# Performance work log

Measured on AMD Instinct MI355X. Metric: run time of the kernel, lower is better.

## Reference

```python
import jax, jax.numpy as jnp
import numpy as np

N, E, IN_C, HID, OUT_C, L = 50000, 800000, 256, 96, 64, 3
DELTAS = (1.0, 0.5, 0.25)


def setup_inputs() -> dict:
    key = jax.random.key(0)
    ks = jax.random.split(key, 10)
    x = jax.random.normal(ks[0], (N, IN_C), dtype=jnp.float32)
    edge_index = jax.random.randint(ks[1], (2, E), 0, N, dtype=jnp.int64)
    s = 1.0 / np.sqrt(IN_C)
    proj_w = jax.random.uniform(ks[2], (IN_C, HID), jnp.float32, -s, s)
    proj_b = jax.random.uniform(ks[3], (HID,), jnp.float32, -s, s)
    sh = 1.0 / np.sqrt(HID)
    conv_w = jax.random.uniform(ks[4], (L, HID, HID), jnp.float32, -sh, sh)
    conv_b = jnp.zeros((L, HID), dtype=jnp.float32)
    so = 1.0 / np.sqrt(2 * HID)
    out_w = jax.random.uniform(ks[5], (2 * HID, OUT_C), jnp.float32, -so, so)
    out_b = jax.random.uniform(ks[6], (OUT_C,), jnp.float32, -so, so)
    # dithered-quantization uniform noise in (-0.5, 0.5), per layer
    b_noise = jax.random.uniform(ks[7], (L, N, HID), jnp.float32) - 0.5
    # additive gaussian noise, per layer
    eps_noise = jax.random.normal(ks[8], (L, N, HID), dtype=jnp.float32) * 0.01
    return {
        "x": x, "edge_index": edge_index,
        "proj_w": proj_w, "proj_b": proj_b,
        "conv_w": conv_w, "conv_b": conv_b,
        "out_w": out_w, "out_b": out_b,
        "b_noise": b_noise, "eps_noise": eps_noise,
    }


def _gcn_norm(edge_index, n):
    # add self-loops and compute symmetric normalization (PyG gcn_norm)
    loops = jnp.arange(n, dtype=edge_index.dtype)
    src = jnp.concatenate([edge_index[0], loops])
    dst = jnp.concatenate([edge_index[1], loops])
    deg = jax.ops.segment_sum(jnp.ones_like(dst, dtype=jnp.float32), dst, num_segments=n)
    dis = jnp.where(deg > 0, jax.lax.rsqrt(jnp.maximum(deg, 1.0)), 0.0)
    norm = dis[src] * dis[dst]  # [E+N]
    return src, dst, norm


def reference(x, edge_index, proj_w, proj_b, conv_w, conv_b, out_w, out_b, b_noise, eps_noise):
    n = x.shape[0]
    src, dst, norm = _gcn_norm(edge_index, n)
    h0 = x @ proj_w + proj_b  # [N, HID]
    h = h0
    for k in range(L):
        delta = DELTAS[k]
        b = b_noise[k] * delta
        h_q = jnp.floor((h + b) / delta) * delta - b  # dithered quantize
        m = h_q @ conv_w[k]                           # [N, HID]
        agg = jax.ops.segment_sum(m[src] * norm[:, None], dst, num_segments=n)
        h = jax.nn.relu(agg + conv_b[k] + eps_noise[k])
    return jnp.concatenate([h0, h], axis=-1) @ out_w + out_b
```

## Files before the change

kernel.cpp:

```cpp
#include <hip/hip_runtime.h>
#include <math.h>

#define N_NODES 50000
#define N_EDGES 800000
#define IN_C    256
#define HID     96
#define OUT_C   64
#define NLAYER  3
#define KC      96
#define XSP     100

#define FMA_ROW(xv, w0, w1, w2, w3, AR) \
    AR[0]=fmaf(xv.x,w0.x,AR[0]); AR[1]=fmaf(xv.x,w0.y,AR[1]); AR[2]=fmaf(xv.x,w0.z,AR[2]); AR[3]=fmaf(xv.x,w0.w,AR[3]); \
    AR[0]=fmaf(xv.y,w1.x,AR[0]); AR[1]=fmaf(xv.y,w1.y,AR[1]); AR[2]=fmaf(xv.y,w1.z,AR[2]); AR[3]=fmaf(xv.y,w1.w,AR[3]); \
    AR[0]=fmaf(xv.z,w2.x,AR[0]); AR[1]=fmaf(xv.z,w2.y,AR[1]); AR[2]=fmaf(xv.z,w2.z,AR[2]); AR[3]=fmaf(xv.z,w2.w,AR[3]); \
    AR[0]=fmaf(xv.w,w3.x,AR[0]); AR[1]=fmaf(xv.w,w3.y,AR[1]); AR[2]=fmaf(xv.w,w3.z,AR[2]); AR[3]=fmaf(xv.w,w3.w,AR[3]);


__global__ void k_init(int* cnt, int* cur, int* counter,
                       int* col, float* wgt, int n) {
    int v = blockIdx.x * blockDim.x + threadIdx.x;
    if (v < n) { cnt[v] = 0; cur[v] = 0; }
    if (v == 0) *counter = 0;
    if (v < 16) { col[N_EDGES + v] = 0; wgt[N_EDGES + v] = 0.f; }
}

__global__ void k_count(const int* __restrict__ ei, int* cnt, int e) {
    int i = blockIdx.x * blockDim.x + threadIdx.x;
    if (i < e) atomicAdd(&cnt[ei[e + i]], 1);
}

__global__ void k_node(const int* __restrict__ cnt, float* __restrict__ dis,
                       int* __restrict__ start, int* counter, int n) {
    int v = blockIdx.x * blockDim.x + threadIdx.x;
    if (v < n) {
        int c = cnt[v];
        dis[v] = (float)(1.0 / sqrt((double)(c + 1)));
        start[v] = atomicAdd(counter, c);
    }
}

__global__ void k_fill(const int* __restrict__ ei, const float* __restrict__ dis,
                       const int* __restrict__ start, int* __restrict__ cur,
                       int* __restrict__ col, float* __restrict__ wgt, int e) {
    int i = blockIdx.x * blockDim.x + threadIdx.x;
    if (i < e) {
        int s = ei[i];
        int d = ei[e + i];
        int slot = start[d] + atomicAdd(&cur[d], 1);
        col[slot] = s;
        wgt[slot] = dis[s] * dis[d];
    }
}


template<bool QUANT, bool BIAS>
__global__ __launch_bounds__(384) void k_gemm(
    const float* __restrict__ A, int lda, int K,
    const float* __restrict__ bn, float delta, float inv_delta,
    const float* __restrict__ W, const float* __restrict__ bias,
    float* __restrict__ C)
{
    __shared__ float xs[64 * XSP];
    const int t  = threadIdx.x;
    const int og = t % 24;
    const int rg = t / 24;
    const int nch = (K + KC - 1) / KC;
    const int ngroups = (N_NODES + 63) / 64;

    const float* Wt = W + 4 * og;

    float4 bv = make_float4(0.f, 0.f, 0.f, 0.f);
    if (BIAS) bv = *(const float4*)&bias[4 * og];

    for (int g = blockIdx.x; g < ngroups; g += gridDim.x) {
        float acc[4][4];
        #pragma unroll
        for (int r = 0; r < 4; r++)
            #pragma unroll
            for (int o = 0; o < 4; o++) acc[r][o] = 0.f;

        for (int ch = 0; ch < nch; ch++) {
            const int kc0 = ch * KC;
            const int kcw = (K - kc0 < KC) ? (K - kc0) : KC;
            const int kq4 = kcw >> 2;
            __syncthreads();
            if (kq4 == 24) {
                float4 va[4], vb[4];
                int nd[4], kq[4];
                #pragma unroll
                for (int j = 0; j < 4; j++) {
                    int i = t + 384 * j;
                    nd[j] = i / 24; kq[j] = i - nd[j] * 24;
                    int gn = g * 64 + nd[j];
                    int gc = gn < N_NODES ? gn : N_NODES - 1;
                    va[j] = *(const float4*)&A[(size_t)gc * lda + kc0 + 4 * kq[j]];
                    if (QUANT)
                        vb[j] = *(const float4*)&bn[(size_t)gc * HID + kc0 + 4 * kq[j]];
                }
                #pragma unroll
                for (int j = 0; j < 4; j++) {
                    float4 v = va[j];
                    if (QUANT) {
                        float bx = vb[j].x * delta, by = vb[j].y * delta;
                        float bz = vb[j].z * delta, bw = vb[j].w * delta;
                        v.x = floorf((v.x + bx) * inv_delta) * delta - bx;
                        v.y = floorf((v.y + by) * inv_delta) * delta - by;
                        v.z = floorf((v.z + bz) * inv_delta) * delta - bz;
                        v.w = floorf((v.w + bw) * inv_delta) * delta - bw;
                    }
                    if (g * 64 + nd[j] >= N_NODES) v = make_float4(0.f, 0.f, 0.f, 0.f);
                    *(float4*)&xs[nd[j] * XSP + 4 * kq[j]] = v;
                }
            } else {
                const int tot = 64 * kq4;
                for (int i = t; i < tot; i += 384) {
                    int node = i >> 4, kq = i & 15;
                    int gn = g * 64 + node;
                    float4 v = make_float4(0.f, 0.f, 0.f, 0.f);
                    if (gn < N_NODES) {
                        v = *(const float4*)&A[(size_t)gn * lda + kc0 + 4 * kq];
                        if (QUANT) {
                            float4 b = *(const float4*)&bn[(size_t)gn * HID + kc0 + 4 * kq];
                            float bx = b.x * delta, by = b.y * delta;
                            float bz = b.z * delta, bw = b.w * delta;
                            v.x = floorf((v.x + bx) * inv_delta) * delta - bx;
                            v.y = floorf((v.y + by) * inv_delta) * delta - by;
                            v.z = floorf((v.z + bz) * inv_delta) * delta - bz;
                            v.w = floorf((v.w + bw) * inv_delta) * delta - bw;
                        }
                    }
                    *(float4*)&xs[node * XSP + 4 * kq] = v;
                }
            }
            __syncthreads();
            const float* Wc = Wt + (size_t)kc0 * HID;
            float4 wa0 = *(const float4*)&Wc[0 * HID];
            float4 wa1 = *(const float4*)&Wc[1 * HID];
            float4 wa2 = *(const float4*)&Wc[2 * HID];
            float4 wa3 = *(const float4*)&Wc[3 * HID];
            for (int k = 0; k < kcw; k += 8) {
                float4 wb0 = *(const float4*)&Wc[(k + 4) * HID];
                float4 wb1 = *(const float4*)&Wc[(k + 5) * HID];
                float4 wb2 = *(const float4*)&Wc[(k + 6) * HID];
                float4 wb3 = *(const float4*)&Wc[(k + 7) * HID];
                #pragma unroll
                for (int r = 0; r < 4; r++) {
                    float4 xv = *(const float4*)&xs[(4 * rg + r) * XSP + k];
                    FMA_ROW(xv, wa0, wa1, wa2, wa3, acc[r]);
                }
                if (k + 8 < kcw) {
                    wa0 = *(const float4*)&Wc[(k + 8)  * HID];
                    wa1 = *(const float4*)&Wc[(k + 9)  * HID];
                    wa2 = *(const float4*)&Wc[(k + 10) * HID];
                    wa3 = *(const float4*)&Wc[(k + 11) * HID];
                }
                #pragma unroll
                for (int r = 0; r < 4; r++) {
                    float4 xv = *(const float4*)&xs[(4 * rg + r) * XSP + k + 4];
                    FMA_ROW(xv, wb0, wb1, wb2, wb3, acc[r]);
                }
            }
        }
        #pragma unroll
        for (int r = 0; r < 4; r++) {
            int gn = g * 64 + 4 * rg + r;
            if (gn < N_NODES) {
                float4 c;
                c.x = acc[r][0] + bv.x;
                c.y = acc[r][1] + bv.y;
                c.z = acc[r][2] + bv.z;
                c.w = acc[r][3] + bv.w;
                *(float4*)&C[(size_t)gn * HID + 4 * og] = c;
            }
        }
    }
}


__global__ __launch_bounds__(384) void k_agg(const float* __restrict__ m,
                                             const int* __restrict__ col,
                                             const float* __restrict__ wgt,
                                             const int* __restrict__ start,
                                             const int* __restrict__ cnt,
                                             const float* __restrict__ dis,
                                             const float* __restrict__ cb,
                                             const float* __restrict__ eps,
                                             float* __restrict__ hout) {
    const int tx = threadIdx.x;
    const int d = blockIdx.x * 4 + threadIdx.y;
    const int s0 = start[d], c = cnt[d];
    const float* mt = m + tx;
    float a[8];
    #pragma unroll
    for (int j = 0; j < 8; j++) a[j] = 0.f;
    for (int e = 0; e < c; e += 16) {
        int   idx[16];
        float wv[16];
        #pragma unroll
        for (int j = 0; j < 16; j++) {
            idx[j] = col[s0 + e + j];
            wv[j]  = (e + j < c) ? wgt[s0 + e + j] : 0.f;
        }
        #pragma unroll
        for (int j = 0; j < 16; j++)
            a[j & 7] = fmaf(mt[idx[j] * HID], wv[j], a[j & 7]);
    }
    float dv = dis[d];
    float s = ((a[0] + a[1]) + (a[2] + a[3])) + ((a[4] + a[5]) + (a[6] + a[7]));
    s = fmaf(mt[d * HID], dv * dv, s);
    s += cb[tx] + eps[(size_t)d * HID + tx];
    hout[(size_t)d * HID + tx] = fmaxf(s, 0.f);
}


__global__ __launch_bounds__(384) void k_out2(const float* __restrict__ h0,
                                              const float* __restrict__ h,
                                              const float* __restrict__ W,
                                              const float* __restrict__ bias,
                                              float* __restrict__ out) {
    __shared__ float xs[96 * XSP];
    const int t  = threadIdx.x;
    const int og = t % 16;
    const int rg = t / 16;
    const int ngroups = (N_NODES + 95) / 96;

    const float* Wt = W + 4 * og;
    float4 bv = *(const float4*)&bias[4 * og];

    for (int g = blockIdx.x; g < ngroups; g += gridDim.x) {
        float acc[4][4];
        #pragma unroll
        for (int r = 0; r < 4; r++)
            #pragma unroll
            for (int o = 0; o < 4; o++) acc[r][o] = 0.f;

        #pragma unroll
        for (int ch = 0; ch < 2; ch++) {
            const float* src = ch ? h : h0;
            __syncthreads();
            float4 va[6];
            int nd[6], kq[6];
            #pragma unroll
            for (int j = 0; j < 6; j++) {
                int i = t + 384 * j;
                nd[j] = i / 24; kq[j] = i - nd[j] * 24;
                int gn = g * 96 + nd[j];
                int gc = gn < N_NODES ? gn : N_NODES - 1;
                va[j] = *(const float4*)&src[(size_t)gc * HID + 4 * kq[j]];
            }
            #pragma unroll
            for (int j = 0; j < 6; j++)
                *(float4*)&xs[nd[j] * XSP + 4 * kq[j]] = va[j];
            __syncthreads();

            const float* Wc = Wt + (size_t)(ch * HID) * OUT_C;
            float4 wa0 = *(const float4*)&Wc[0 * OUT_C];
            float4 wa1 = *(const float4*)&Wc[1 * OUT_C];
            float4 wa2 = *(const float4*)&Wc[2 * OUT_C];
            float4 wa3 = *(const float4*)&Wc[3 * OUT_C];
            for (int k = 0; k < HID; k += 8) {
                float4 wb0 = *(const float4*)&Wc[(k + 4) * OUT_C];
                float4 wb1 = *(const float4*)&Wc[(k + 5) * OUT_C];
                float4 wb2 = *(const float4*)&Wc[(k + 6) * OUT_C];
                float4 wb3 = *(const float4*)&Wc[(k + 7) * OUT_C];
                #pragma unroll
                for (int r = 0; r < 4; r++) {
                    float4 xv = *(const float4*)&xs[(4 * rg + r) * XSP + k];
                    FMA_ROW(xv, wa0, wa1, wa2, wa3, acc[r]);
                }
                if (k + 8 < HID) {
                    wa0 = *(const float4*)&Wc[(k + 8)  * OUT_C];
                    wa1 = *(const float4*)&Wc[(k + 9)  * OUT_C];
                    wa2 = *(const float4*)&Wc[(k + 10) * OUT_C];
                    wa3 = *(const float4*)&Wc[(k + 11) * OUT_C];
                }
                #pragma unroll
                for (int r = 0; r < 4; r++) {
                    float4 xv = *(const float4*)&xs[(4 * rg + r) * XSP + k + 4];
                    FMA_ROW(xv, wb0, wb1, wb2, wb3, acc[r]);
                }
            }
        }
        #pragma unroll
        for (int r = 0; r < 4; r++) {
            int gn = g * 96 + 4 * rg + r;
            if (gn < N_NODES) {
                float4 c;
                c.x = acc[r][0] + bv.x;
                c.y = acc[r][1] + bv.y;
                c.z = acc[r][2] + bv.z;
                c.w = acc[r][3] + bv.w;
                *(float4*)&out[(size_t)gn * OUT_C + 4 * og] = c;
            }
        }
    }
}


extern "C" void kernel_launch(void* const* d_in, const int* in_sizes, int n_in,
                              void* d_out, int out_size, void* d_ws, size_t ws_size,
                              hipStream_t stream) {
    (void)in_sizes; (void)n_in; (void)out_size; (void)ws_size;
    const float* x       = (const float*)d_in[0];
    const int*   ei      = (const int*)d_in[1];
    const float* proj_w  = (const float*)d_in[2];
    const float* proj_b  = (const float*)d_in[3];
    const float* conv_w  = (const float*)d_in[4];
    const float* conv_b  = (const float*)d_in[5];
    const float* out_w   = (const float*)d_in[6];
    const float* out_b   = (const float*)d_in[7];
    const float* b_noise = (const float*)d_in[8];
    const float* eps_n   = (const float*)d_in[9];
    float*       out     = (float*)d_out;

    char* w = (char*)d_ws;
    size_t off = 0;
    auto alloc = [&](size_t bytes) -> char* {
        char* p = w + off;
        off = (off + bytes + 255) & ~(size_t)255;
        return p;
    };
    float* h0b   = (float*)alloc((size_t)N_NODES * HID * 4);
    float* hA    = (float*)alloc((size_t)N_NODES * HID * 4);
    float* mb    = (float*)alloc((size_t)N_NODES * HID * 4);
    float* dis   = (float*)alloc((size_t)N_NODES * 4);
    float* wgt   = (float*)alloc((size_t)(N_EDGES + 16) * 4);
    int*   col   = (int*)  alloc((size_t)(N_EDGES + 16) * 4);
    int*   cnt   = (int*)  alloc((size_t)N_NODES * 4);
    int*   cur   = (int*)  alloc((size_t)N_NODES * 4);
    int*   start = (int*)  alloc((size_t)N_NODES * 4);
    int*   ctr   = (int*)  alloc(256);

    k_init <<<(N_NODES + 255) / 256, 256, 0, stream>>>(cnt, cur, ctr, col, wgt, N_NODES);
    k_count<<<(N_EDGES + 255) / 256, 256, 0, stream>>>(ei, cnt, N_EDGES);
    k_node <<<(N_NODES + 255) / 256, 256, 0, stream>>>(cnt, dis, start, ctr, N_NODES);
    k_fill <<<(N_EDGES + 255) / 256, 256, 0, stream>>>(ei, dis, start, cur, col, wgt, N_EDGES);

    const int ngroups = (N_NODES + 63) / 64;

    k_gemm<false, true><<<ngroups, 384, 0, stream>>>(
        x, IN_C, IN_C, nullptr, 1.f, 1.f, proj_w, proj_b, h0b);

    const float deltas[NLAYER] = {1.0f, 0.5f, 0.25f};
    const float* hprev = h0b;
    for (int k = 0; k < NLAYER; k++) {
        float dlt = deltas[k];
        k_gemm<true, false><<<ngroups, 384, 0, stream>>>(
            hprev, HID, HID,
            b_noise + (size_t)k * N_NODES * HID, dlt, 1.0f / dlt,
            conv_w + (size_t)k * HID * HID, nullptr, mb);
        k_agg<<<N_NODES / 4, dim3(96, 4), 0, stream>>>(
            mb, col, wgt, start, cnt, dis,
            conv_b + (size_t)k * HID,
            eps_n + (size_t)k * N_NODES * HID, hA);
        hprev = hA;
    }

    const int ogroups = (N_NODES + 95) / 96;
    k_out2<<<ogroups, 384, 0, stream>>>(h0b, hprev, out_w, out_b, out);
}
```

Measured before the change: 670.1 us.

## Fuse aggregation with per-layer GEMM and move quantization into producer epilogues

```diff
diff --git a/kernel.cpp b/kernel.cpp
--- a/kernel.cpp
+++ b/kernel.cpp
@@ -54,12 +54,14 @@
 }
 
 
-template<bool QUANT, bool BIAS>
+template<bool QUANT, bool BIAS, bool QOUT>
 __global__ __launch_bounds__(384) void k_gemm(
     const float* __restrict__ A, int lda, int K,
     const float* __restrict__ bn, float delta, float inv_delta,
     const float* __restrict__ W, const float* __restrict__ bias,
-    float* __restrict__ C)
+    float* __restrict__ C,
+    const float* __restrict__ bnq, float dq, float inv_dq,
+    float* __restrict__ Cq)
 {
     __shared__ float xs[64 * XSP];
     const int t  = threadIdx.x;
@@ -172,45 +174,131 @@
                 c.z = acc[r][2] + bv.z;
                 c.w = acc[r][3] + bv.w;
                 *(float4*)&C[(size_t)gn * HID + 4 * og] = c;
-            }
-        }
-    }
-}
-
-
-__global__ __launch_bounds__(384) void k_agg(const float* __restrict__ m,
-                                             const int* __restrict__ col,
-                                             const float* __restrict__ wgt,
-                                             const int* __restrict__ start,
-                                             const int* __restrict__ cnt,
-                                             const float* __restrict__ dis,
-                                             const float* __restrict__ cb,
-                                             const float* __restrict__ eps,
-                                             float* __restrict__ hout) {
-    const int tx = threadIdx.x;
-    const int d = blockIdx.x * 4 + threadIdx.y;
-    const int s0 = start[d], c = cnt[d];
-    const float* mt = m + tx;
-    float a[8];
+                if (QOUT) {
+                    float4 b = *(const float4*)&bnq[(size_t)gn * HID + 4 * og];
+                    float bx = b.x * dq, by = b.y * dq;
+                    float bz = b.z * dq, bw = b.w * dq;
+                    float4 q;
+                    q.x = floorf((c.x + bx) * inv_dq) * dq - bx;
+                    q.y = floorf((c.y + by) * inv_dq) * dq - by;
+                    q.z = floorf((c.z + bz) * inv_dq) * dq - bz;
+                    q.w = floorf((c.w + bw) * inv_dq) * dq - bw;
+                    *(float4*)&Cq[(size_t)gn * HID + 4 * og] = q;
+                }
+            }
+        }
+    }
+}
+
+
+__global__ __launch_bounds__(384) void k_layer(
+    const float* __restrict__ hq,
+    const int* __restrict__ col, const float* __restrict__ wgt,
+    const int* __restrict__ start, const int* __restrict__ cnt,
+    const float* __restrict__ dis,
+    const float* __restrict__ W,
+    const float* __restrict__ cb,
+    const float* __restrict__ eps,
+    const float* __restrict__ bnq, float dq, float inv_dq,
+    float* __restrict__ hout, int quant_out)
+{
+    __shared__ float sg[64 * XSP];
+    const int t = threadIdx.x;
+    const int g = blockIdx.x;
+
+    {
+        const int tx = t % 96;
+        const int ty = t / 96;
+        const float* ht = hq + tx;
+        for (int i = 0; i < 16; i++) {
+            int ld = ty * 16 + i;
+            int d  = g * 64 + ld;
+            float s = 0.f;
+            if (d < N_NODES) {
+                int s0 = start[d], c = cnt[d];
+                float a[8];
+                #pragma unroll
+                for (int j = 0; j < 8; j++) a[j] = 0.f;
+                for (int e = 0; e < c; e += 16) {
+                    int   idx[16];
+                    float wv[16];
+                    #pragma unroll
+                    for (int j = 0; j < 16; j++) {
+                        idx[j] = col[s0 + e + j];
+                        wv[j]  = (e + j < c) ? wgt[s0 + e + j] : 0.f;
+                    }
+                    #pragma unroll
+                    for (int j = 0; j < 16; j++)
+                        a[j & 7] = fmaf(ht[idx[j] * HID], wv[j], a[j & 7]);
+                }
+                float dv = dis[d];
+                s = ((a[0] + a[1]) + (a[2] + a[3])) + ((a[4] + a[5]) + (a[6] + a[7]));
+                s = fmaf(ht[d * HID], dv * dv, s);
+            }
+            sg[ld * XSP + tx] = s;
+        }
+    }
+    __syncthreads();
+
+    const int og = t % 24;
+    const int rg = t / 24;
+    const float* Wt = W + 4 * og;
+    float acc[4][4];
     #pragma unroll
-    for (int j = 0; j < 8; j++) a[j] = 0.f;
-    for (int e = 0; e < c; e += 16) {
-        int   idx[16];
-        float wv[16];
-        #pragma unroll
-        for (int j = 0; j < 16; j++) {
-            idx[j] = col[s0 + e + j];
-            wv[j]  = (e + j < c) ? wgt[s0 + e + j] : 0.f;
-        }
-        #pragma unroll
-        for (int j = 0; j < 16; j++)
-            a[j & 7] = fmaf(mt[idx[j] * HID], wv[j], a[j & 7]);
-    }
-    float dv = dis[d];
-    float s = ((a[0] + a[1]) + (a[2] + a[3])) + ((a[4] + a[5]) + (a[6] + a[7]));
-    s = fmaf(mt[d * HID], dv * dv, s);
-    s += cb[tx] + eps[(size_t)d * HID + tx];
-    hout[(size_t)d * HID + tx] = fmaxf(s, 0.f);
+    for (int r = 0; r < 4; r++)
+        #pragma unroll
+        for (int o = 0; o < 4; o++) acc[r][o] = 0.f;
+
+    float4 wa0 = *(const float4*)&Wt[0 * HID];
+    float4 wa1 = *(const float4*)&Wt[1 * HID];
+    float4 wa2 = *(const float4*)&Wt[2 * HID];
+    float4 wa3 = *(const float4*)&Wt[3 * HID];
+    for (int k = 0; k < HID; k += 8) {
+        float4 wb0 = *(const float4*)&Wt[(k + 4) * HID];
+        float4 wb1 = *(const float4*)&Wt[(k + 5) * HID];
+        float4 wb2 = *(const float4*)&Wt[(k + 6) * HID];
+        float4 wb3 = *(const float4*)&Wt[(k + 7) * HID];
+        #pragma unroll
+        for (int r = 0; r < 4; r++) {
+            float4 xv = *(const float4*)&sg[(4 * rg + r) * XSP + k];
+            FMA_ROW(xv, wa0, wa1, wa2, wa3, acc[r]);
+        }
+        if (k + 8 < HID) {
+            wa0 = *(const float4*)&Wt[(k + 8)  * HID];
+            wa1 = *(const float4*)&Wt[(k + 9)  * HID];
+            wa2 = *(const float4*)&Wt[(k + 10) * HID];
+            wa3 = *(const float4*)&Wt[(k + 11) * HID];
+        }
+        #pragma unroll
+        for (int r = 0; r < 4; r++) {
+            float4 xv = *(const float4*)&sg[(4 * rg + r) * XSP + k + 4];
+            FMA_ROW(xv, wb0, wb1, wb2, wb3, acc[r]);
+        }
+    }
+
+    float4 bv = *(const float4*)&cb[4 * og];
+    #pragma unroll
+    for (int r = 0; r < 4; r++) {
+        int gn = g * 64 + 4 * rg + r;
+        if (gn < N_NODES) {
+            float4 ev = *(const float4*)&eps[(size_t)gn * HID + 4 * og];
+            float4 h;
+            h.x = fmaxf(acc[r][0] + bv.x + ev.x, 0.f);
+            h.y = fmaxf(acc[r][1] + bv.y + ev.y, 0.f);
+            h.z = fmaxf(acc[r][2] + bv.z + ev.z, 0.f);
+            h.w = fmaxf(acc[r][3] + bv.w + ev.w, 0.f);
+            if (quant_out) {
+                float4 b = *(const float4*)&bnq[(size_t)gn * HID + 4 * og];
+                float bx = b.x * dq, by = b.y * dq;
+                float bz = b.z * dq, bw = b.w * dq;
+                h.x = floorf((h.x + bx) * inv_dq) * dq - bx;
+                h.y = floorf((h.y + by) * inv_dq) * dq - by;
+                h.z = floorf((h.z + bz) * inv_dq) * dq - bz;
+                h.w = floorf((h.w + bw) * inv_dq) * dq - bw;
+            }
+            *(float4*)&hout[(size_t)gn * HID + 4 * og] = h;
+        }
+    }
 }
 
 
@@ -323,7 +411,8 @@
     };
     float* h0b   = (float*)alloc((size_t)N_NODES * HID * 4);
     float* hA    = (float*)alloc((size_t)N_NODES * HID * 4);
-    float* mb    = (float*)alloc((size_t)N_NODES * HID * 4);
+    float* hqA   = (float*)alloc((size_t)N_NODES * HID * 4);
+    float* hqB   = (float*)alloc((size_t)N_NODES * HID * 4);
     float* dis   = (float*)alloc((size_t)N_NODES * 4);
     float* wgt   = (float*)alloc((size_t)(N_EDGES + 16) * 4);
     int*   col   = (int*)  alloc((size_t)(N_EDGES + 16) * 4);
@@ -338,25 +427,28 @@
     k_fill <<<(N_EDGES + 255) / 256, 256, 0, stream>>>(ei, dis, start, cur, col, wgt, N_EDGES);
 
     const int ngroups = (N_NODES + 63) / 64;
-
-    k_gemm<false, true><<<ngroups, 384, 0, stream>>>(
-        x, IN_C, IN_C, nullptr, 1.f, 1.f, proj_w, proj_b, h0b);
-
     const float deltas[NLAYER] = {1.0f, 0.5f, 0.25f};
-    const float* hprev = h0b;
+
+    k_gemm<false, true, true><<<ngroups, 384, 0, stream>>>(
+        x, IN_C, IN_C, nullptr, 1.f, 1.f, proj_w, proj_b, h0b,
+        b_noise, deltas[0], 1.0f / deltas[0], hqA);
+
+    const float* hin = hqA;
     for (int k = 0; k < NLAYER; k++) {
-        float dlt = deltas[k];
-        k_gemm<true, false><<<ngroups, 384, 0, stream>>>(
-            hprev, HID, HID,
-            b_noise + (size_t)k * N_NODES * HID, dlt, 1.0f / dlt,
-            conv_w + (size_t)k * HID * HID, nullptr, mb);
-        k_agg<<<N_NODES / 4, dim3(96, 4), 0, stream>>>(
-            mb, col, wgt, start, cnt, dis,
+        int lastl = (k == NLAYER - 1);
+        float dn = lastl ? 1.f : deltas[k + 1];
+        float* ho = lastl ? hA : (hin == hqA ? hqB : hqA);
+        k_layer<<<ngroups, 384, 0, stream>>>(
+            hin, col, wgt, start, cnt, dis,
+            conv_w + (size_t)k * HID * HID,
             conv_b + (size_t)k * HID,
-            eps_n + (size_t)k * N_NODES * HID, hA);
-        hprev = hA;
+            eps_n + (size_t)k * N_NODES * HID,
+            lastl ? nullptr : b_noise + (size_t)(k + 1) * N_NODES * HID,
+            dn, 1.0f / dn,
+            ho, lastl ? 0 : 1);
+        hin = ho;
     }
 
     const int ogroups = (N_NODES + 95) / 96;
-    k_out2<<<ogroups, 384, 0, stream>>>(h0b, hprev, out_w, out_b, out);
-}
+    k_out2<<<ogroups, 384, 0, stream>>>(h0b, hA, out_w, out_b, out);
+}
```

New measurement: 748.6 us. 1.12x slower.
